# Kernel tuning notes

Hardware: AMD Instinct MI355X
Metric: run time of the kernel (lower is better)

## Reference

```python
import jax, jax.numpy as jnp
import numpy as np

B, N, L, VALID_Y = 1, 3072, 256, 200
DIM_X, DIM_Y, H = 3072, 1536, 24
HD = DIM_X // H  # 128
EPS_MOD, EPS_RMS = 1e-6, 1e-5


def _mod_rmsnorm(t, scale):
    # F.rms_norm (no weight) then modulate by (1 + scale)
    tn = t * jax.lax.rsqrt(jnp.mean(t * t, axis=-1, keepdims=True) + EPS_MOD)
    return tn * (1.0 + scale[:, None, :])


def _rmsnorm(t, w):
    return t * jax.lax.rsqrt(jnp.mean(t * t, axis=-1, keepdims=True) + EPS_RMS) * w


def _rope(t, cos, sin):
    # t: (B, N, H, HD); cos/sin: (N, H, HD/2); even/odd interleaved rotary
    te, to = t[..., 0::2], t[..., 1::2]
    cp = te * cos - to * sin
    sp = te * sin + to * cos
    return jnp.stack([cp, sp], axis=-1).reshape(t.shape)


def setup_inputs() -> dict:
    key = jax.random.key(0)
    ks = jax.random.split(key, 12)
    s = 0.02
    d = {}
    d['x'] = jax.random.normal(ks[0], (B, N, DIM_X), jnp.float32)
    d['y'] = jax.random.normal(ks[1], (B, L, DIM_Y), jnp.float32)
    d['scale_x'] = jax.random.normal(ks[2], (B, DIM_X), jnp.float32) * 0.1
    d['scale_y'] = jax.random.normal(ks[3], (B, DIM_Y), jnp.float32) * 0.1
    ang = jax.random.uniform(ks[4], (N, H, HD // 2), jnp.float32, 0.0, 2.0 * np.pi)
    d['rope_cos'] = jnp.cos(ang)
    d['rope_sin'] = jnp.sin(ang)
    d['W_qkv_x'] = jax.random.normal(ks[5], (DIM_X, 3 * DIM_X), jnp.float32) * s
    d['b_qkv_x'] = jnp.zeros((3 * DIM_X,), jnp.float32)
    d['W_qkv_y'] = jax.random.normal(ks[6], (DIM_Y, 3 * DIM_X), jnp.float32) * s
    d['b_qkv_y'] = jnp.zeros((3 * DIM_X,), jnp.float32)
    d['w_qn_x'] = jnp.ones((HD,), jnp.float32)
    d['w_kn_x'] = jnp.ones((HD,), jnp.float32)
    d['w_qn_y'] = jnp.ones((HD,), jnp.float32)
    d['w_kn_y'] = jnp.ones((HD,), jnp.float32)
    d['W_proj_x'] = jax.random.normal(ks[7], (DIM_X, DIM_X), jnp.float32) * s
    d['b_proj_x'] = jnp.zeros((DIM_X,), jnp.float32)
    d['W_proj_y'] = jax.random.normal(ks[8], (DIM_X, DIM_Y), jnp.float32) * s
    d['b_proj_y'] = jnp.zeros((DIM_Y,), jnp.float32)
    # B=1 packing: all N video tokens + first VALID_Y text tokens of flattened (N+L)
    d['valid_token_indices'] = jnp.arange(N + VALID_Y, dtype=jnp.int32)
    return d


def reference(x, y, scale_x, scale_y, rope_cos, rope_sin,
              W_qkv_x, b_qkv_x, W_qkv_y, b_qkv_y,
              w_qn_x, w_kn_x, w_qn_y, w_kn_y,
              W_proj_x, b_proj_x, W_proj_y, b_proj_y,
              valid_token_indices):
    # ---- visual stream: modulated RMSNorm -> qkv -> qk-norm -> RoPE ----
    xm = _mod_rmsnorm(x, scale_x)
    qkv_x = (xm @ W_qkv_x + b_qkv_x).reshape(B, N, 3, H, HD)
    qkv_x = jnp.transpose(qkv_x, (2, 0, 1, 3, 4))  # (3,B,N,H,HD)
    q_x, k_x, v_x = qkv_x[0], qkv_x[1], qkv_x[2]
    q_x = _rope(_rmsnorm(q_x, w_qn_x), rope_cos, rope_sin)
    k_x = _rope(_rmsnorm(k_x, w_kn_x), rope_cos, rope_sin)
    # ---- text stream: modulated RMSNorm -> qkv -> qk-norm ----
    ym = _mod_rmsnorm(y, scale_y)
    qkv_y = (ym @ W_qkv_y + b_qkv_y).reshape(B, L, 3, H, HD)
    q_y, k_y, v_y = qkv_y[:, :, 0], qkv_y[:, :, 1], qkv_y[:, :, 2]
    q_y = _rmsnorm(q_y, w_qn_y)
    k_y = _rmsnorm(k_y, w_kn_y)
    # ---- unify_streams: concat, pack, gather valid tokens ----
    qkv = jnp.stack([
        jnp.concatenate([q_x, q_y], axis=1),
        jnp.concatenate([k_x, k_y], axis=1),
        jnp.concatenate([v_x, v_y], axis=1),
    ], axis=2).reshape(B * (N + L), 3, H, HD)
    qkv = qkv[valid_token_indices]  # (total, 3, H, HD)
    q, k, v = qkv[:, 0], qkv[:, 1], qkv[:, 2]
    # ---- varlen attention (B=1 -> single segment, full attention) ----
    scale = 1.0 / np.sqrt(HD)
    scores = jnp.einsum('qhd,khd->hqk', q, k) * scale
    attn = jax.nn.softmax(scores, axis=-1)
    out = jnp.einsum('hqk,khd->qhd', attn, v).reshape(-1, H * HD)  # (total, DIM_X)
    # ---- pad_and_split_xy: scatter back to padded stream, split ----
    padded = jnp.zeros((B * (N + L), H * HD), out.dtype).at[valid_token_indices].set(out)
    padded = padded.reshape(B, N + L, H * HD)
    x_out = padded[:, :N] @ W_proj_x + b_proj_x
    y_out = padded[:, N:] @ W_proj_y + b_proj_y
    return (x_out, y_out)
```

## Files before the change

### kernel.cpp

```cpp
#include <hip/hip_runtime.h>


typedef short short8 __attribute__((ext_vector_type(8)));
typedef float f32x4 __attribute__((ext_vector_type(4)));
typedef unsigned short ushort4v __attribute__((ext_vector_type(4)));

#define MFMA_BF16(a,b,c) __builtin_amdgcn_mfma_f32_16x16x32_bf16((a),(b),(c),0,0,0)

#define NH 24
#define SPAD 3328
#define SVAL 3272

__device__ __forceinline__ unsigned short bf16_rne(float f){
  unsigned int u = __builtin_bit_cast(unsigned int, f);
  u += 0x7FFFu + ((u >> 16) & 1u);
  return (unsigned short)(u >> 16);
}
__device__ __forceinline__ float bf2f(unsigned short h){
  unsigned int u = ((unsigned int)h) << 16;
  return __builtin_bit_cast(float, u);
}
__device__ __forceinline__ void gload16(const void* g, void* l){
  __builtin_amdgcn_global_load_lds(
      (const __attribute__((address_space(1))) unsigned int*)g,
      (__attribute__((address_space(3))) unsigned int*)l, 16, 0, 0);
}

__global__ __launch_bounds__(256) void transpose_w(
    const float* __restrict__ W, unsigned short* __restrict__ Wt, int K, int N)
{
  __shared__ unsigned short t[64][66];
  int n0 = blockIdx.x*64, k0 = blockIdx.y*64;
  int tid = threadIdx.x;
  int kr = tid >> 4, nc = (tid & 15) * 4;
  #pragma unroll
  for (int pass=0; pass<4; pass++){
    int k = kr + pass*16;
    float4 v = *(const float4*)(W + (size_t)(k0+k)*N + n0 + nc);
    ushort4v o;
    o.x = bf16_rne(v.x); o.y = bf16_rne(v.y);
    o.z = bf16_rne(v.z); o.w = bf16_rne(v.w);
    *(ushort4v*)&t[k][nc] = o;
  }
  __syncthreads();
  int nr = tid >> 3, kc = (tid & 7) * 8;
  #pragma unroll
  for (int pass=0; pass<2; pass++){
    int n = nr + pass*32;
    unsigned short buf[8];
    #pragma unroll
    for (int j=0;j<8;j++) buf[j] = t[kc+j][n];
    *(short8*)(Wt + (size_t)(n0+n)*K + k0 + kc) = *(short8*)&buf[0];
  }
}

template<int D>
__global__ __launch_bounds__(256) void modnorm(
    const float* __restrict__ X, const float* __restrict__ scale,
    unsigned short* __restrict__ out)
{
  int row = blockIdx.x;
  const float4* xv = (const float4*)(X + (size_t)row*D);
  float ss = 0.f;
  for (int i = threadIdx.x; i < D/4; i += 256){
    float4 v = xv[i];
    ss += v.x*v.x + v.y*v.y + v.z*v.z + v.w*v.w;
  }
  #pragma unroll
  for (int d=1; d<64; d<<=1) ss += __shfl_xor(ss, d);
  __shared__ float wsum[4];
  if ((threadIdx.x & 63) == 0) wsum[threadIdx.x >> 6] = ss;
  __syncthreads();
  float tot = wsum[0] + wsum[1] + wsum[2] + wsum[3];
  float rn = rsqrtf(tot*(1.0f/(float)D) + 1e-6f);
  const float4* sv = (const float4*)scale;
  for (int i = threadIdx.x; i < D/4; i += 256){
    float4 v = xv[i]; float4 s4 = sv[i];
    ushort4v o;
    o.x = bf16_rne(v.x*rn*(1.f+s4.x));
    o.y = bf16_rne(v.y*rn*(1.f+s4.y));
    o.z = bf16_rne(v.z*rn*(1.f+s4.z));
    o.w = bf16_rne(v.w*rn*(1.f+s4.w));
    *(ushort4v*)(out + (size_t)row*D + i*4) = o;
  }
}

template<typename CT, bool BIAS>
__global__ __launch_bounds__(256, 3) void gemm_bt(
    const unsigned short* __restrict__ A, const unsigned short* __restrict__ BT,
    const float* __restrict__ bias, CT* __restrict__ C,
    int M, int N, int K, int ldc, int klen)
{
  __shared__ unsigned short lA[128*32];
  __shared__ unsigned short lB[128*32];
  int tid = threadIdx.x, wave = tid>>6, lane = tid&63;
  int l16 = lane&15, g = lane>>4;
  int wr = wave>>1, wc = wave&1;

  int nwg = gridDim.x*gridDim.y;
  int orig = blockIdx.y*gridDim.x + blockIdx.x;
  int neo = orig;
  if ((nwg & 7) == 0){
    int q8 = nwg >> 3;
    neo = (orig & 7)*q8 + (orig >> 3);
  }
  int bx = neo / gridDim.y;
  int by = neo % gridDim.y;
  int bm = by*128, bn = bx*128;
  int kof = blockIdx.z * klen;
  CT* Cp = C + (size_t)blockIdx.z * M * (size_t)ldc;

  f32x4 acc[4][4] = {};

  for (int k0 = kof; k0 < kof + klen; k0 += 32){
    #pragma unroll
    for (int i=0;i<2;i++){
      int off = i*4096 + wave*1024 + lane*16;
      int row = off>>6;
      int sp  = (off>>4)&3;
      int sk  = (sp ^ (row&3))*8;
      gload16(A + (size_t)(bm+row)*K + k0 + sk, (char*)lA + i*4096 + wave*1024);
    }
    #pragma unroll
    for (int i=0;i<2;i++){
      int off = i*4096 + wave*1024 + lane*16;
      int row = off>>6;
      int sp  = (off>>4)&3;
      int sk  = (sp ^ (row&3))*8;
      gload16(BT + (size_t)(bn+row)*K + k0 + sk, (char*)lB + i*4096 + wave*1024);
    }
    __syncthreads();

    short8 a[4], b[4];
    #pragma unroll
    for (int m=0;m<4;m++){
      int row = wr*64 + m*16 + l16;
      int slot = g ^ (row&3);
      a[m] = *(const short8*)((const char*)lA + row*64 + slot*16);
    }
    #pragma unroll
    for (int n=0;n<4;n++){
      int row = wc*64 + n*16 + l16;
      int slot = g ^ (row&3);
      b[n] = *(const short8*)((const char*)lB + row*64 + slot*16);
    }
    __builtin_amdgcn_s_setprio(1);
    #pragma unroll
    for (int m=0;m<4;m++)
      #pragma unroll
      for (int n=0;n<4;n++)
        acc[m][n] = MFMA_BF16(a[m], b[n], acc[m][n]);
    __builtin_amdgcn_s_setprio(0);
    __syncthreads();
  }

  #pragma unroll
  for (int n=0;n<4;n++){
    int col = bn + wc*64 + n*16 + l16;
    float bv = BIAS ? bias[col] : 0.f;
    #pragma unroll
    for (int m=0;m<4;m++){
      int row0 = bm + wr*64 + m*16 + g*4;
      #pragma unroll
      for (int r=0;r<4;r++){
        float v = acc[m][n][r] + bv;
        if constexpr (sizeof(CT) == 4) Cp[(size_t)(row0+r)*ldc + col] = v;
        else                           Cp[(size_t)(row0+r)*ldc + col] = bf16_rne(v);
      }
    }
  }
}

__global__ __launch_bounds__(512, 2) void gemm_8ph(
    const unsigned short* __restrict__ A, const unsigned short* __restrict__ BT,
    const float* __restrict__ bias, unsigned short* __restrict__ C,
    int M, int N, int K, int ldc)
{
  __shared__ unsigned short lds[8][8192];

  int tid = threadIdx.x, wave = tid>>6, lane = tid&63;
  int l16 = lane&15, g = lane>>4;
  int wr = wave>>2, wc = wave&3;

  int nwg = gridDim.x*gridDim.y;
  int orig = blockIdx.y*gridDim.x + blockIdx.x;
  int neo = orig;
  if ((nwg & 7) == 0) neo = (orig & 7)*(nwg>>3) + (orig>>3);
  int bx = neo / gridDim.y, by = neo % gridDim.y;
  int bm = by*256, bn = bx*256;

  const int NT = K >> 6;

  auto STAGE = [&](int t, int op, int half, int b){
    int tc = t < NT ? t : NT-1;
    const unsigned short* src = op ? BT : A;
    int base_row = (op ? bn : bm) + half*128;
    int k0 = tc << 6;
    #pragma unroll
    for (int j=0;j<2;j++){
      int o = (j*8 + wave)*1024 + lane*16;
      int row = o>>7, slot = (o>>4)&7;
      int sk = (slot ^ (row&7))*8;
      gload16(src + (size_t)(base_row+row)*K + k0 + sk,
              (char*)&lds[(b<<2)|(op<<1)|half][0] + (j*8+wave)*1024);
    }
  };

  short8 afr[4], bfr[8];
  auto LDA = [&](int b, int p){
    const char* basep = (const char*)&lds[(b<<2)|wr][0];
    #pragma unroll
    for (int mm=0;mm<2;mm++){
      int row = (p*2+mm)*16 + l16;
      #pragma unroll
      for (int kk=0;kk<2;kk++)
        afr[mm*2+kk] = *(const short8*)(basep + row*128 + (((kk*4+g) ^ (row&7))<<4));
    }
  };
  auto LDB = [&](int b){
    const char* basep = (const char*)&lds[(b<<2)|2|(wc>>1)][0];
    int rbase = (wc&1)*64;
    #pragma unroll
    for (int n=0;n<4;n++){
      int row = rbase + n*16 + l16;
      #pragma unroll
      for (int kk=0;kk<2;kk++)
        bfr[n*2+kk] = *(const short8*)(basep + row*128 + (((kk*4+g) ^ (row&7))<<4));
    }
  };

  f32x4 acc[8][4] = {};

  STAGE(0,1,0,0); STAGE(0,1,1,0); STAGE(0,0,0,0); STAGE(0,0,1,0);
  STAGE(1,1,0,1); STAGE(1,1,1,1); STAGE(1,0,0,1);
  asm volatile("s_waitcnt vmcnt(6)" ::: "memory");
  __builtin_amdgcn_s_barrier();

  int NIT = NT >> 1;
  for (int i=0;i<NIT;i++){
    int T = 2*i;
    #pragma unroll
    for (int p=0;p<4;p++){
      if (p==0) LDB(0);
      LDA(0, p);
      if (p==0)      STAGE(T+1,0,1,1);
      else if (p==1) STAGE(T+2,1,0,0);
      else if (p==2) STAGE(T+2,1,1,0);
      else           STAGE(T+2,0,0,0);
      if (p==0) asm volatile("s_waitcnt lgkmcnt(8)" ::: "memory");
      __builtin_amdgcn_s_barrier();
      asm volatile("s_waitcnt lgkmcnt(0)" ::: "memory");
      __builtin_amdgcn_sched_barrier(0);
      __builtin_amdgcn_s_setprio(1);
      #pragma unroll
      for (int mm=0;mm<2;mm++)
        #pragma unroll
        for (int n=0;n<4;n++)
          #pragma unroll
          for (int kk=0;kk<2;kk++)
            acc[p*2+mm][n] = MFMA_BF16(afr[mm*2+kk], bfr[n*2+kk], acc[p*2+mm][n]);
      __builtin_amdgcn_s_setprio(0);
      if (p==3) asm volatile("s_waitcnt vmcnt(6)" ::: "memory");
      __builtin_amdgcn_s_barrier();
    }
    #pragma unroll
    for (int p=0;p<4;p++){
      if (p==0) LDB(1);
      LDA(1, p);
      if (p==0)      STAGE(T+2,0,1,0);
      else if (p==1) STAGE(T+3,1,0,1);
      else if (p==2) STAGE(T+3,1,1,1);
      else           STAGE(T+3,0,0,1);
      if (p==0) asm volatile("s_waitcnt lgkmcnt(8)" ::: "memory");
      __builtin_amdgcn_s_barrier();
      asm volatile("s_waitcnt lgkmcnt(0)" ::: "memory");
      __builtin_amdgcn_sched_barrier(0);
      __builtin_amdgcn_s_setprio(1);
      #pragma unroll
      for (int mm=0;mm<2;mm++)
        #pragma unroll
        for (int n=0;n<4;n++)
          #pragma unroll
          for (int kk=0;kk<2;kk++)
            acc[p*2+mm][n] = MFMA_BF16(afr[mm*2+kk], bfr[n*2+kk], acc[p*2+mm][n]);
      __builtin_amdgcn_s_setprio(0);
      if (p==3) asm volatile("s_waitcnt vmcnt(6)" ::: "memory");
      __builtin_amdgcn_s_barrier();
    }
  }

  #pragma unroll
  for (int n=0;n<4;n++){
    int col = bn + wc*64 + n*16 + l16;
    float bv = bias[col];
    #pragma unroll
    for (int m=0;m<8;m++){
      int row0 = bm + wr*128 + m*16 + g*4;
      #pragma unroll
      for (int r=0;r<4;r++)
        C[(size_t)(row0+r)*ldc + col] = bf16_rne(acc[m][n][r] + bv);
    }
  }
}

__global__ __launch_bounds__(256) void reduce2_bias_bf16(
    const float* __restrict__ part, const float* __restrict__ bias,
    unsigned short* __restrict__ out, int N, size_t tot)
{
  size_t idx = ((size_t)blockIdx.x*256 + threadIdx.x)*4;
  if (idx >= tot) return;
  float4 a = *(const float4*)(part + idx);
  float4 b = *(const float4*)(part + tot + idx);
  int col = (int)(idx % N);
  float4 bv = *(const float4*)(bias + col);
  ushort4v o;
  o.x = bf16_rne(a.x+b.x+bv.x);
  o.y = bf16_rne(a.y+b.y+bv.y);
  o.z = bf16_rne(a.z+b.z+bv.z);
  o.w = bf16_rne(a.w+b.w+bv.w);
  *(ushort4v*)(out + idx) = o;
}

__global__ __launch_bounds__(256) void reduce8_bias_f32(
    const float* __restrict__ part, const float* __restrict__ bias,
    float* __restrict__ out, int N, size_t tot)
{
  size_t idx = ((size_t)blockIdx.x*256 + threadIdx.x)*4;
  if (idx >= tot) return;
  int col = (int)(idx % N);
  float4 s = *(const float4*)(bias + col);
  #pragma unroll
  for (int c=0;c<8;c++){
    float4 a = *(const float4*)(part + (size_t)c*tot + idx);
    s.x += a.x; s.y += a.y; s.z += a.z; s.w += a.w;
  }
  *(float4*)(out + idx) = s;
}

__global__ __launch_bounds__(256) void fixup_qk(
    const unsigned short* __restrict__ QKV,
    const float* __restrict__ cosT, const float* __restrict__ sinT,
    const float* __restrict__ wqx, const float* __restrict__ wkx,
    const float* __restrict__ wqy, const float* __restrict__ wky,
    unsigned short* __restrict__ Qo, unsigned short* __restrict__ Ko)
{
  int wave = threadIdx.x >> 6, lane = threadIdx.x & 63;
  int bid = blockIdx.x*4 + wave;
  int t = bid / NH, h = bid % NH;
  bool isx = (t < 3072);

  const unsigned short* base = QKV + (size_t)t*9216 + h*128;
  unsigned int qraw = *(const unsigned int*)(base + 2*lane);
  unsigned int kraw = *(const unsigned int*)(base + 3072 + 2*lane);
  float q0 = bf2f((unsigned short)(qraw & 0xffff)), q1 = bf2f((unsigned short)(qraw >> 16));
  float k0 = bf2f((unsigned short)(kraw & 0xffff)), k1 = bf2f((unsigned short)(kraw >> 16));

  float sq = q0*q0 + q1*q1, sk = k0*k0 + k1*k1;
  #pragma unroll
  for (int d=1; d<64; d<<=1){ sq += __shfl_xor(sq, d); sk += __shfl_xor(sk, d); }
  float rq = rsqrtf(sq*(1.0f/128.0f) + 1e-5f);
  float rk = rsqrtf(sk*(1.0f/128.0f) + 1e-5f);

  const float* wq = isx ? wqx : wqy;
  const float* wk = isx ? wkx : wky;
  float a0 = q0*rq*wq[2*lane], a1 = q1*rq*wq[2*lane+1];
  float b0 = k0*rk*wk[2*lane], b1 = k1*rk*wk[2*lane+1];

  if (isx){
    size_t ci = ((size_t)t*NH + h)*64 + lane;
    float c = cosT[ci], s = sinT[ci];
    float t0 = a0*c - a1*s, t1 = a0*s + a1*c; a0 = t0; a1 = t1;
    t0 = b0*c - b1*s; t1 = b0*s + b1*c; b0 = t0; b1 = t1;
  }
  size_t oi = ((size_t)h*SPAD + t)*128 + 2*lane;
  *(unsigned int*)(Qo + oi) = (unsigned int)bf16_rne(a0) | ((unsigned int)bf16_rne(a1) << 16);
  *(unsigned int*)(Ko + oi) = (unsigned int)bf16_rne(b0) | ((unsigned int)bf16_rne(b1) << 16);
}

__global__ __launch_bounds__(256) void v_transpose(
    const unsigned short* __restrict__ QKV, unsigned short* __restrict__ VT)
{
  __shared__ unsigned short t[64][136];
  int h = blockIdx.x;
  int t0 = blockIdx.y*64;
  int tid = threadIdx.x;
  #pragma unroll
  for (int it=0; it<4; it++){
    int chunk = it*256 + tid;
    int r = chunk >> 4, c = chunk & 15;
    short8 v = *(const short8*)(QKV + (size_t)(t0 + r)*9216 + 6144 + h*128 + c*8);
    *(short8*)&t[r][c*8] = v;
  }
  __syncthreads();
  int d = tid >> 1, half = tid & 1;
  size_t ob = (size_t)(h*128 + d)*SPAD + t0 + half*32;
  #pragma unroll
  for (int j=0;j<32;j+=2){
    unsigned int v = (unsigned int)t[half*32 + j][d] | ((unsigned int)t[half*32 + j + 1][d] << 16);
    *(unsigned int*)(VT + ob + j) = v;
  }
}

__global__ __launch_bounds__(256, 3) void attn_fwd(
    const unsigned short* __restrict__ Q, const unsigned short* __restrict__ Kb,
    const unsigned short* __restrict__ VT, unsigned short* __restrict__ O)
{
  __shared__ unsigned short lK[2][32*128];
  __shared__ unsigned short lV[2][128*32];
  __shared__ unsigned short lP[4][32*72];

  int tid = threadIdx.x, wave = tid>>6, lane = tid&63;
  int l16 = lane&15, g = lane>>4;
  int h = blockIdx.x, qt = blockIdx.y;
  int q0 = qt*128 + wave*32;

  auto STAGE = [&](int kt, int b){
    #pragma unroll
    for (int i=0;i<2;i++){
      int off = (i*4 + wave)*1024 + lane*16;
      int row = off>>8;
      int sp  = (off>>4)&15;
      int ssp = sp ^ (row&7);
      gload16(Kb + ((size_t)h*SPAD + kt*32 + row)*128 + ssp*8,
              (char*)&lK[b][0] + (i*4 + wave)*1024);
    }
    #pragma unroll
    for (int i=0;i<2;i++){
      int off = (i*4 + wave)*1024 + lane*16;
      int row = off>>6;
      int sp  = (off>>4)&3;
      int ssp = sp ^ (row&3);
      gload16(VT + ((size_t)(h*128 + row))*SPAD + kt*32 + ssp*8,
              (char*)&lV[b][0] + (i*4 + wave)*1024);
    }
  };

  short8 qf[2][4];
  const unsigned short* qbase = Q + (size_t)h*SPAD*128;
  #pragma unroll
  for (int mt=0;mt<2;mt++){
    int row = q0 + mt*16 + l16;
    #pragma unroll
    for (int ks=0;ks<4;ks++)
      qf[mt][ks] = *(const short8*)(qbase + (size_t)row*128 + ks*32 + g*8);
  }

  f32x4 oacc[2][8] = {};
  float lsum[2][4] = {};

  unsigned short* lPw = &lP[wave][0];
  const float sc = 0.08838834764831845f;

  STAGE(0, 0);

  for (int kt=0; kt<104; kt++){
    int cur = kt & 1;
    int nxt = (kt+1 < 104) ? kt+1 : 103;
    STAGE(nxt, cur ^ 1);
    asm volatile("s_waitcnt vmcnt(4)" ::: "memory");
    __builtin_amdgcn_s_barrier();

    const char* lKc = (const char*)&lK[cur][0];
    const char* lVc = (const char*)&lV[cur][0];

    f32x4 s[2][2] = {};
    #pragma unroll
    for (int ks=0;ks<4;ks++){
      short8 bfrag[2];
      #pragma unroll
      for (int nt=0;nt<2;nt++){
        int row = nt*16 + l16;
        int slot = (ks*4 + g) ^ (row&7);
        bfrag[nt] = *(const short8*)(lKc + row*256 + slot*16);
      }
      __builtin_amdgcn_s_setprio(1);
      #pragma unroll
      for (int mt=0;mt<2;mt++)
        #pragma unroll
        for (int nt=0;nt<2;nt++)
          s[mt][nt] = MFMA_BF16(qf[mt][ks], bfrag[nt], s[mt][nt]);
      __builtin_amdgcn_s_setprio(0);
    }

    bool edge = (kt >= 102);
    #pragma unroll
    for (int mt=0;mt<2;mt++)
      #pragma unroll
      for (int nt=0;nt<2;nt++){
        int key = kt*32 + nt*16 + l16;
        bool msk = edge && (key >= SVAL);
        #pragma unroll
        for (int r=0;r<4;r++){
          float p = __expf(fmaf(s[mt][nt][r], sc, -12.f));
          p = msk ? 0.f : p;
          lsum[mt][r] += p;
          lPw[(mt*16 + g*4 + r)*72 + nt*16 + l16] = bf16_rne(p);
        }
      }

    asm volatile("s_waitcnt lgkmcnt(0)" ::: "memory");

    {
      short8 pa[2];
      #pragma unroll
      for (int mt=0;mt<2;mt++)
        pa[mt] = *(const short8*)(lPw + (mt*16 + l16)*72 + g*8);
      __builtin_amdgcn_s_setprio(1);
      #pragma unroll
      for (int dt=0;dt<8;dt++){
        int row = dt*16 + l16;
        int slot = g ^ (row&3);
        short8 vb = *(const short8*)(lVc + row*64 + slot*16);
        #pragma unroll
        for (int mt=0;mt<2;mt++)
          oacc[mt][dt] = MFMA_BF16(pa[mt], vb, oacc[mt][dt]);
      }
      __builtin_amdgcn_s_setprio(0);
    }
    __builtin_amdgcn_s_barrier();
  }

  #pragma unroll
  for (int mt=0;mt<2;mt++){
    float inv[4];
    #pragma unroll
    for (int r=0;r<4;r++){
      float v = lsum[mt][r];
      v += __shfl_xor(v, 1); v += __shfl_xor(v, 2);
      v += __shfl_xor(v, 4); v += __shfl_xor(v, 8);
      inv[r] = 1.0f / v;
    }
    #pragma unroll
    for (int dt=0;dt<8;dt++)
      #pragma unroll
      for (int r=0;r<4;r++){
        int row = q0 + mt*16 + g*4 + r;
        if (row < SVAL)
          O[(size_t)row*3072 + h*128 + dt*16 + l16] = bf16_rne(oacc[mt][dt][r]*inv[r]);
      }
  }
}

static const size_t OFF_WT_QKV_X  = 0;
static const size_t OFF_WT_QKV_Y  = 56623104;
static const size_t OFF_WT_PROJ_X = 84934656;
static const size_t OFF_WT_PROJ_Y = 103809024;
static const size_t OFF_XM        = 113246208;
static const size_t OFF_YM        = 132120576;
static const size_t OFF_QKV       = 132907008;
static const size_t OFF_Q         = 194248704;
static const size_t OFF_K         = 214695936;
static const size_t OFF_VT        = 235143168;
static const size_t WS_NEEDED     = 255590400;
static const size_t OFF_AO        = 0;

extern "C" void kernel_launch(void* const* d_in, const int* in_sizes, int n_in,
                              void* d_out, int out_size, void* d_ws, size_t ws_size,
                              hipStream_t stream) {
  if (ws_size < WS_NEEDED) return;

  const float* x        = (const float*)d_in[0];
  const float* y        = (const float*)d_in[1];
  const float* scale_x  = (const float*)d_in[2];
  const float* scale_y  = (const float*)d_in[3];
  const float* rope_cos = (const float*)d_in[4];
  const float* rope_sin = (const float*)d_in[5];
  const float* W_qkv_x  = (const float*)d_in[6];
  const float* b_qkv_x  = (const float*)d_in[7];
  const float* W_qkv_y  = (const float*)d_in[8];
  const float* b_qkv_y  = (const float*)d_in[9];
  const float* w_qn_x   = (const float*)d_in[10];
  const float* w_kn_x   = (const float*)d_in[11];
  const float* w_qn_y   = (const float*)d_in[12];
  const float* w_kn_y   = (const float*)d_in[13];
  const float* W_proj_x = (const float*)d_in[14];
  const float* b_proj_x = (const float*)d_in[15];
  const float* W_proj_y = (const float*)d_in[16];
  const float* b_proj_y = (const float*)d_in[17];

  float* out_x = (float*)d_out;
  float* out_y = out_x + (size_t)3072*3072;

  char* ws = (char*)d_ws;
  unsigned short* Wt_qkv_x  = (unsigned short*)(ws + OFF_WT_QKV_X);
  unsigned short* Wt_qkv_y  = (unsigned short*)(ws + OFF_WT_QKV_Y);
  unsigned short* Wt_proj_x = (unsigned short*)(ws + OFF_WT_PROJ_X);
  unsigned short* Wt_proj_y = (unsigned short*)(ws + OFF_WT_PROJ_Y);
  unsigned short* xm        = (unsigned short*)(ws + OFF_XM);
  unsigned short* ym        = (unsigned short*)(ws + OFF_YM);
  unsigned short* qkv       = (unsigned short*)(ws + OFF_QKV);
  unsigned short* Qb        = (unsigned short*)(ws + OFF_Q);
  unsigned short* Kb        = (unsigned short*)(ws + OFF_K);
  unsigned short* VTb       = (unsigned short*)(ws + OFF_VT);
  unsigned short* attnout   = (unsigned short*)(ws + OFF_AO);
  float* part_qkv_y         = (float*)(ws + OFF_XM);
  float* part_proj_y        = (float*)(ws + OFF_Q);

  transpose_w<<<dim3(9216/64, 3072/64), 256, 0, stream>>>(W_qkv_x,  Wt_qkv_x,  3072, 9216);
  transpose_w<<<dim3(9216/64, 1536/64), 256, 0, stream>>>(W_qkv_y,  Wt_qkv_y,  1536, 9216);
  transpose_w<<<dim3(3072/64, 3072/64), 256, 0, stream>>>(W_proj_x, Wt_proj_x, 3072, 3072);
  transpose_w<<<dim3(1536/64, 3072/64), 256, 0, stream>>>(W_proj_y, Wt_proj_y, 3072, 1536);

  modnorm<3072><<<3072, 256, 0, stream>>>(x, scale_x, xm);
  modnorm<1536><<<256,  256, 0, stream>>>(y, scale_y, ym);

  gemm_8ph<<<dim3(36, 12), 512, 0, stream>>>(
      xm, Wt_qkv_x, b_qkv_x, qkv, 3072, 9216, 3072, 9216);

  gemm_bt<float, false><<<dim3(72, 2, 2), 256, 0, stream>>>(
      ym, Wt_qkv_y, nullptr, part_qkv_y, 256, 9216, 1536, 9216, 768);
  reduce2_bias_bf16<<<2304, 256, 0, stream>>>(
      part_qkv_y, b_qkv_y, qkv + (size_t)3072*9216, 9216, (size_t)256*9216);

  fixup_qk<<<SVAL*NH/4, 256, 0, stream>>>(qkv, rope_cos, rope_sin,
                                          w_qn_x, w_kn_x, w_qn_y, w_kn_y, Qb, Kb);
  v_transpose<<<dim3(NH, SPAD/64), 256, 0, stream>>>(qkv, VTb);

  (void)hipMemsetAsync(attnout + (size_t)SVAL*3072, 0,
                       (size_t)(SPAD - SVAL)*3072*2, stream);

  attn_fwd<<<dim3(NH, SPAD/128), 256, 0, stream>>>(Qb, Kb, VTb, attnout);

  gemm_bt<float, true><<<dim3(24, 24, 1), 256, 0, stream>>>(
      attnout, Wt_proj_x, b_proj_x, out_x, 3072, 3072, 3072, 3072, 3072);

  gemm_bt<float, false><<<dim3(12, 2, 8), 256, 0, stream>>>(
      attnout + (size_t)3072*3072, Wt_proj_y, nullptr, part_proj_y,
      256, 1536, 3072, 1536, 384);
  reduce8_bias_f32<<<384, 256, 0, stream>>>(
      part_proj_y, b_proj_y, out_y, 1536, (size_t)256*1536);
}
```

Before: 608.8 us.

## Use hardware packed bf16 conversion, exp2 softmax, and new V LDS swizzle

Replaces the software round-to-nearest-even bf16 conversion with the v_cvt_pk_bf16_f32 instruction in every kernel that packs bf16 output. In attention, it folds log2(e) into the scale so exp2f is used directly, and it restructures masking so edge tiles alone pay the compare. It also changes the V tile XOR swizzle to use (row>>1)&3, consistently on both the write and read side, to reduce LDS bank conflicts. The aim is fewer ALU instructions in the softmax/P-store path and fewer conflicting LDS reads for V.

```diff
diff --git a/kernel.cpp b/kernel.cpp
--- a/kernel.cpp
+++ b/kernel.cpp
@@ -20,6 +20,11 @@
   unsigned int u = ((unsigned int)h) << 16;
   return __builtin_bit_cast(float, u);
 }
+__device__ __forceinline__ unsigned int cvt_pk_bf16(float lo, float hi){
+  unsigned int r;
+  asm("v_cvt_pk_bf16_f32 %0, %1, %2" : "=v"(r) : "v"(lo), "v"(hi));
+  return r;
+}
 __device__ __forceinline__ void gload16(const void* g, void* l){
   __builtin_amdgcn_global_load_lds(
       (const __attribute__((address_space(1))) unsigned int*)g,
@@ -37,10 +42,10 @@
   for (int pass=0; pass<4; pass++){
     int k = kr + pass*16;
     float4 v = *(const float4*)(W + (size_t)(k0+k)*N + n0 + nc);
-    ushort4v o;
-    o.x = bf16_rne(v.x); o.y = bf16_rne(v.y);
-    o.z = bf16_rne(v.z); o.w = bf16_rne(v.w);
-    *(ushort4v*)&t[k][nc] = o;
+    unsigned int u01 = cvt_pk_bf16(v.x, v.y);
+    unsigned int u23 = cvt_pk_bf16(v.z, v.w);
+    *(unsigned int*)&t[k][nc]   = u01;
+    *(unsigned int*)&t[k][nc+2] = u23;
   }
   __syncthreads();
   int nr = tid >> 3, kc = (tid & 7) * 8;
@@ -76,12 +81,10 @@
   const float4* sv = (const float4*)scale;
   for (int i = threadIdx.x; i < D/4; i += 256){
     float4 v = xv[i]; float4 s4 = sv[i];
-    ushort4v o;
-    o.x = bf16_rne(v.x*rn*(1.f+s4.x));
-    o.y = bf16_rne(v.y*rn*(1.f+s4.y));
-    o.z = bf16_rne(v.z*rn*(1.f+s4.z));
-    o.w = bf16_rne(v.w*rn*(1.f+s4.w));
-    *(ushort4v*)(out + (size_t)row*D + i*4) = o;
+    unsigned int u01 = cvt_pk_bf16(v.x*rn*(1.f+s4.x), v.y*rn*(1.f+s4.y));
+    unsigned int u23 = cvt_pk_bf16(v.z*rn*(1.f+s4.z), v.w*rn*(1.f+s4.w));
+    uint2 o = {u01, u23};
+    *(uint2*)(out + (size_t)row*D + i*4) = o;
   }
 }
 
@@ -313,12 +316,10 @@
   float4 b = *(const float4*)(part + tot + idx);
   int col = (int)(idx % N);
   float4 bv = *(const float4*)(bias + col);
-  ushort4v o;
-  o.x = bf16_rne(a.x+b.x+bv.x);
-  o.y = bf16_rne(a.y+b.y+bv.y);
-  o.z = bf16_rne(a.z+b.z+bv.z);
-  o.w = bf16_rne(a.w+b.w+bv.w);
-  *(ushort4v*)(out + idx) = o;
+  unsigned int u01 = cvt_pk_bf16(a.x+b.x+bv.x, a.y+b.y+bv.y);
+  unsigned int u23 = cvt_pk_bf16(a.z+b.z+bv.z, a.w+b.w+bv.w);
+  uint2 o = {u01, u23};
+  *(uint2*)(out + idx) = o;
 }
 
 __global__ __launch_bounds__(256) void reduce8_bias_f32(
@@ -373,8 +374,8 @@
     t0 = b0*c - b1*s; t1 = b0*s + b1*c; b0 = t0; b1 = t1;
   }
   size_t oi = ((size_t)h*SPAD + t)*128 + 2*lane;
-  *(unsigned int*)(Qo + oi) = (unsigned int)bf16_rne(a0) | ((unsigned int)bf16_rne(a1) << 16);
-  *(unsigned int*)(Ko + oi) = (unsigned int)bf16_rne(b0) | ((unsigned int)bf16_rne(b1) << 16);
+  *(unsigned int*)(Qo + oi) = cvt_pk_bf16(a0, a1);
+  *(unsigned int*)(Ko + oi) = cvt_pk_bf16(b0, b1);
 }
 
 __global__ __launch_bounds__(256) void v_transpose(
@@ -429,7 +430,7 @@
       int off = (i*4 + wave)*1024 + lane*16;
       int row = off>>6;
       int sp  = (off>>4)&3;
-      int ssp = sp ^ (row&3);
+      int ssp = sp ^ ((row>>1)&3);
       gload16(VT + ((size_t)(h*128 + row))*SPAD + kt*32 + ssp*8,
               (char*)&lV[b][0] + (i*4 + wave)*1024);
     }
@@ -449,7 +450,8 @@
   float lsum[2][4] = {};
 
   unsigned short* lPw = &lP[wave][0];
-  const float sc = 0.08838834764831845f;
+  const float sc2 = 0.08838834764831845f * 1.4426950408889634f;
+  const float C2  = -12.0f * 1.4426950408889634f;
 
   STAGE(0, 0);
 
@@ -487,14 +489,19 @@
     for (int mt=0;mt<2;mt++)
       #pragma unroll
       for (int nt=0;nt<2;nt++){
-        int key = kt*32 + nt*16 + l16;
-        bool msk = edge && (key >= SVAL);
         #pragma unroll
-        for (int r=0;r<4;r++){
-          float p = __expf(fmaf(s[mt][nt][r], sc, -12.f));
-          p = msk ? 0.f : p;
-          lsum[mt][r] += p;
-          lPw[(mt*16 + g*4 + r)*72 + nt*16 + l16] = bf16_rne(p);
+        for (int r=0;r<4;r+=2){
+          float p0 = exp2f(fmaf(s[mt][nt][r],   sc2, C2));
+          float p1 = exp2f(fmaf(s[mt][nt][r+1], sc2, C2));
+          if (edge){
+            int key = kt*32 + nt*16 + l16;
+            if (key >= SVAL){ p0 = 0.f; p1 = 0.f; }
+          }
+          lsum[mt][r]   += p0;
+          lsum[mt][r+1] += p1;
+          unsigned int pk = cvt_pk_bf16(p0, p1);
+          lPw[(mt*16 + g*4 + r  )*72 + nt*16 + l16] = (unsigned short)pk;
+          lPw[(mt*16 + g*4 + r+1)*72 + nt*16 + l16] = (unsigned short)(pk >> 16);
         }
       }
 
@@ -509,7 +516,7 @@
       #pragma unroll
       for (int dt=0;dt<8;dt++){
         int row = dt*16 + l16;
-        int slot = g ^ (row&3);
+        int slot = g ^ ((row>>1)&3);
         short8 vb = *(const short8*)(lVc + row*64 + slot*16);
         #pragma unroll
         for (int mt=0;mt<2;mt++)
```

After: 622.0 us. 1.02x slower.
